# Kernel tuning notes

Hardware: AMD Instinct MI355X
Metric: run time of the kernel (lower is better)

## Reference

```python
import jax, jax.numpy as jnp
import numpy as np
from jax.scipy.linalg import expm

LATENT, HID, OMEGA, TRANZ, K = 64, 40, 9, 3, 262144


def _linear_params(key, out_d, in_d):
    # equinox Linear default init: U(-1/sqrt(in), 1/sqrt(in)) for weight and bias
    lim = 1.0 / np.sqrt(in_d)
    kw, kb = jax.random.split(key)
    W = jax.random.uniform(kw, (out_d, in_d), minval=-lim, maxval=lim, dtype=jnp.float32)
    b = jax.random.uniform(kb, (out_d,), minval=-lim, maxval=lim, dtype=jnp.float32)
    return W, b


def setup_inputs() -> dict:
    key = jax.random.key(0)
    keys = jax.random.split(key, 7)
    W_o1, b_o1 = _linear_params(keys[0], HID, LATENT)
    W_o2, b_o2 = _linear_params(keys[1], HID, HID)
    W_o3, b_o3 = _linear_params(keys[2], OMEGA, HID)
    W_t1, b_t1 = _linear_params(keys[3], HID, LATENT)
    W_t2, b_t2 = _linear_params(keys[4], HID, HID)
    W_t3, b_t3 = _linear_params(keys[5], TRANZ, HID)
    x = jax.random.normal(keys[6], (LATENT, K), dtype=jnp.float32)
    return {
        "x": x,
        "W_o1": W_o1, "b_o1": b_o1, "W_o2": W_o2, "b_o2": b_o2, "W_o3": W_o3, "b_o3": b_o3,
        "W_t1": W_t1, "b_t1": b_t1, "W_t2": W_t2, "b_t2": b_t2, "W_t3": W_t3, "b_t3": b_t3,
    }


def _exp_omega(omega_flat):
    # omega_flat: (9, K); expm of each column reshaped to 3x3, flattened -> (K, 9)
    f = lambda col: expm(col.reshape(3, 3)).reshape(9)
    return jax.vmap(f, in_axes=1)(omega_flat)


def reference(x, W_o1, b_o1, W_o2, b_o2, W_o3, b_o3,
              W_t1, b_t1, W_t2, b_t2, W_t3, b_t3):
    relu = jax.nn.relu
    # omega branch (note: original applies relu after EVERY layer, incl. last)
    h = relu(W_o1 @ x + b_o1[:, None])
    h = relu(W_o2 @ h + b_o2[:, None])
    omega = relu(W_o3 @ h + b_o3[:, None])          # (9, K)
    rotation = _exp_omega(omega).T                   # (9, K)
    # translation branch
    t = relu(W_t1 @ x + b_t1[:, None])
    t = relu(W_t2 @ t + b_t2[:, None])
    translation = relu(W_t3 @ t + b_t3[:, None])     # (3, K)
    return (omega, rotation, translation)
```

## Files before the change

### kernel.cpp

```cpp
#include <hip/hip_runtime.h>
#include <hip/hip_bf16.h>

#define KC 262144

typedef __attribute__((ext_vector_type(8))) short bf16x8;
typedef __attribute__((ext_vector_type(4))) float f32x4;
typedef unsigned short u16;
typedef unsigned int u32;

__device__ __forceinline__ u16 f2bf(float f) {
    u32 u = __float_as_uint(f);
    return (u16)((u + 0x7fffu + ((u >> 16) & 1u)) >> 16);
}
__device__ __forceinline__ u32 pk2(float a, float b) {
    u16 lo = __bfloat16_as_ushort(__float2bfloat16(a));
    u16 hi = __bfloat16_as_ushort(__float2bfloat16(b));
    return (u32)lo | ((u32)hi << 16);
}
__device__ __forceinline__ float bf2f(u32 h) {
    return __uint_as_float(h << 16);
}

__global__ __launch_bounds__(256) void prep(
    const float* __restrict__ Wo1, const float* __restrict__ bo1,
    const float* __restrict__ Wo2, const float* __restrict__ bo2,
    const float* __restrict__ Wo3, const float* __restrict__ bo3,
    const float* __restrict__ Wt1, const float* __restrict__ bt1,
    const float* __restrict__ Wt2, const float* __restrict__ bt2,
    const float* __restrict__ Wt3, const float* __restrict__ bt3,
    u16* __restrict__ ws)
{
    u16* W1s = ws;
    u16* W2s = ws + 5120;
    u16* W3s = ws + 12800;
    float* b1s = (float*)(ws + 14336);
    const int t0 = blockIdx.x * 256 + threadIdx.x;
    const int NT = gridDim.x * 256;

    for (int i = t0; i < 5120; i += NT) {
        int r = i >> 6, k = i & 63;
        float v = (r < 40) ? Wo1[r * 64 + k] : Wt1[(r - 40) * 64 + k];
        W1s[i] = f2bf(v);
    }
    for (int i = t0; i < 7680; i += NT) {
        int r = i / 96, k = i - r * 96;
        float v = 0.f;
        if (r < 40) {
            if (k < 40) v = Wo2[r * 40 + k];
            else if (k == 80) v = bo2[r];
        } else {
            int rr = r - 40;
            if (k >= 40 && k < 80) v = Wt2[rr * 40 + (k - 40)];
            else if (k == 80) v = bt2[rr];
        }
        W2s[i] = f2bf(v);
    }
    for (int i = t0; i < 1536; i += NT) {
        int r = i / 96, k = i - r * 96;
        float v = 0.f;
        if (r < 9) {
            if (k < 40) v = Wo3[r * 40 + k];
            else if (k == 80) v = bo3[r];
        } else if (r < 12) {
            int rr = r - 9;
            if (k >= 40 && k < 80) v = Wt3[rr * 40 + (k - 40)];
            else if (k == 80) v = bt3[rr];
        }
        W3s[i] = f2bf(v);
    }
    for (int i = t0; i < 80; i += NT)
        b1s[i] = (i < 40) ? bo1[i] : bt1[i - 40];
}

__device__ __forceinline__ void transpose_h(
    const u32* Px, const u32* Py, int g, int c, bf16x8* hb)
{
    const int srcA = 16 * (2 * (g & 1)) + c;
    const int srcB = srcA + 16;
    const bool hiM = (g >= 2);
#pragma unroll
    for (int s = 0; s < 2; ++s) {
        union { u32 u[4]; bf16x8 v; } uu;
        u32 a0 = (u32)__shfl((int)Px[2 * s], srcA);
        u32 b0 = (u32)__shfl((int)Px[2 * s + 1], srcA);
        uu.u[0] = hiM ? b0 : a0;
        u32 a1 = (u32)__shfl((int)Py[2 * s], srcA);
        u32 b1 = (u32)__shfl((int)Py[2 * s + 1], srcA);
        uu.u[1] = hiM ? b1 : a1;
        u32 a2 = (u32)__shfl((int)Px[2 * s], srcB);
        u32 b2 = (u32)__shfl((int)Px[2 * s + 1], srcB);
        uu.u[2] = hiM ? b2 : a2;
        u32 a3 = (u32)__shfl((int)Py[2 * s], srcB);
        u32 b3 = (u32)__shfl((int)Py[2 * s + 1], srcB);
        uu.u[3] = hiM ? b3 : a3;
        hb[s] = uu.v;
    }
    {
        union { u32 u[4]; bf16x8 v; } uu;
        u32 v0 = (u32)__shfl((int)Px[4], srcA);
        u32 v1 = (u32)__shfl((int)Py[4], srcA);
        u32 v2 = (u32)__shfl((int)Px[4], srcB);
        u32 v3 = (u32)__shfl((int)Py[4], srcB);
        u32 k0 = (g == 2) ? 0x00003f80u : 0u;
        uu.u[0] = hiM ? k0 : v0;
        uu.u[1] = hiM ? 0u : v1;
        uu.u[2] = hiM ? 0u : v2;
        uu.u[3] = hiM ? 0u : v3;
        hb[2] = uu.v;
    }
}

__global__ __launch_bounds__(256, 1) void mlp_shfl(
    const float* __restrict__ x, const u16* __restrict__ ws,
    float* __restrict__ out)
{
    const u16* W1s = ws;
    const u16* W2s = ws + 5120;
    const u16* W3s = ws + 12800;
    const float* b1s = (const float*)(ws + 14336);

    const int tid = threadIdx.x;
    const int wid = tid >> 6;
    const int lane = tid & 63;
    const int g = lane >> 4;
    const int c = lane & 15;
    const int wgid = blockIdx.x * 4 + wid;
    const int cbase = wgid * 64;

    bf16x8 A1[5][2], A3[3];
    f32x4 b1v[5];
#pragma unroll
    for (int m = 0; m < 5; ++m) {
#pragma unroll
        for (int s = 0; s < 2; ++s)
            A1[m][s] = *(const bf16x8*)(W1s + (16 * m + c) * 64 + 32 * s + 8 * g);
        b1v[m] = *(const f32x4*)(b1s + 16 * m + 4 * g);
    }
    bf16x8 A2[5][3];
#pragma unroll
    for (int m = 0; m < 5; ++m)
#pragma unroll
        for (int s = 0; s < 3; ++s)
            if (!(s == 0 && m >= 3))
                A2[m][s] = *(const bf16x8*)(W2s + (16 * m + c) * 96 + 32 * s + 8 * g);
#pragma unroll
    for (int s = 0; s < 3; ++s)
        A3[s] = *(const bf16x8*)(W3s + c * 96 + 32 * s + 8 * g);

    u32 xoff[16];
#pragma unroll
    for (int jj = 0; jj < 16; ++jj) {
        int row = 8 * g + (jj & 7) + 32 * (jj >> 3);
        xoff[jj] = (u32)((row * KC + cbase + c) * 4);
    }
    const char* xb_ = (const char*)x;

    float xr[16];
#pragma unroll
    for (int jj = 0; jj < 16; ++jj)
        xr[jj] = *(const float*)(xb_ + xoff[jj]);

    u32 w0[4], w1[4];

#pragma unroll
    for (int t = 0; t < 4; ++t) {
        bf16x8 xv[2];
#pragma unroll
        for (int s = 0; s < 2; ++s) {
            union { u32 u[4]; bf16x8 v; } uu;
#pragma unroll
            for (int p = 0; p < 4; ++p)
                uu.u[p] = pk2(xr[8 * s + 2 * p], xr[8 * s + 2 * p + 1]);
            xv[s] = uu.v;
        }

        float xrn[16];
        if (t < 3) {
#pragma unroll
            for (int jj = 0; jj < 16; ++jj)
                xrn[jj] = *(const float*)(xb_ + (xoff[jj] + (t + 1) * 64));
        }

        f32x4 a1[5];
#pragma unroll
        for (int m = 0; m < 5; ++m) a1[m] = b1v[m];
#pragma unroll
        for (int s = 0; s < 2; ++s)
#pragma unroll
            for (int m = 0; m < 5; ++m)
                a1[m] = __builtin_amdgcn_mfma_f32_16x16x32_bf16(
                    A1[m][s], xv[s], a1[m], 0, 0, 0);

        u32 Px[5], Py[5];
#pragma unroll
        for (int m = 0; m < 5; ++m) {
            Px[m] = pk2(fmaxf(a1[m][0], 0.f), fmaxf(a1[m][1], 0.f));
            Py[m] = pk2(fmaxf(a1[m][2], 0.f), fmaxf(a1[m][3], 0.f));
        }
        bf16x8 hb[3];
        transpose_h(Px, Py, g, c, hb);

        f32x4 a2[5];
#pragma unroll
        for (int m = 0; m < 5; ++m) a2[m] = f32x4{0.f, 0.f, 0.f, 0.f};
#pragma unroll
        for (int s = 0; s < 3; ++s)
#pragma unroll
            for (int m = 0; m < 5; ++m)
                if (!(s == 0 && m >= 3))
                    a2[m] = __builtin_amdgcn_mfma_f32_16x16x32_bf16(
                        A2[m][s], hb[s], a2[m], 0, 0, 0);
#pragma unroll
        for (int m = 0; m < 5; ++m) {
            Px[m] = pk2(fmaxf(a2[m][0], 0.f), fmaxf(a2[m][1], 0.f));
            Py[m] = pk2(fmaxf(a2[m][2], 0.f), fmaxf(a2[m][3], 0.f));
        }
        transpose_h(Px, Py, g, c, hb);

        f32x4 a3 = f32x4{0.f, 0.f, 0.f, 0.f};
#pragma unroll
        for (int s = 0; s < 3; ++s)
            a3 = __builtin_amdgcn_mfma_f32_16x16x32_bf16(
                A3[s], hb[s], a3, 0, 0, 0);

        w0[t] = pk2(fmaxf(a3[0], 0.f), fmaxf(a3[1], 0.f));
        w1[t] = pk2(fmaxf(a3[2], 0.f), fmaxf(a3[3], 0.f));

        if (t < 3) {
#pragma unroll
            for (int jj = 0; jj < 16; ++jj)
                xr[jj] = xrn[jj];
        }
    }

    {
        const int T = lane >> 4;
        const int cp = lane & 15;
        const int s0 = cp, s1 = 16 + cp, s2 = 32 + cp;

        auto selT = [&](u32 v0, u32 v1, u32 v2, u32 v3) -> u32 {
            u32 lo = (T & 1) ? v1 : v0;
            u32 hi = (T & 1) ? v3 : v2;
            return (T & 2) ? hi : lo;
        };
        u32 q0 = selT((u32)__shfl((int)w0[0], s0), (u32)__shfl((int)w0[1], s0),
                      (u32)__shfl((int)w0[2], s0), (u32)__shfl((int)w0[3], s0));
        u32 q1 = selT((u32)__shfl((int)w1[0], s0), (u32)__shfl((int)w1[1], s0),
                      (u32)__shfl((int)w1[2], s0), (u32)__shfl((int)w1[3], s0));
        u32 q2 = selT((u32)__shfl((int)w0[0], s1), (u32)__shfl((int)w0[1], s1),
                      (u32)__shfl((int)w0[2], s1), (u32)__shfl((int)w0[3], s1));
        u32 q3 = selT((u32)__shfl((int)w1[0], s1), (u32)__shfl((int)w1[1], s1),
                      (u32)__shfl((int)w1[2], s1), (u32)__shfl((int)w1[3], s1));
        u32 q4 = selT((u32)__shfl((int)w0[0], s2), (u32)__shfl((int)w0[1], s2),
                      (u32)__shfl((int)w0[2], s2), (u32)__shfl((int)w0[3], s2));
        u32 q5 = selT((u32)__shfl((int)w1[0], s2), (u32)__shfl((int)w1[1], s2),
                      (u32)__shfl((int)w1[2], s2), (u32)__shfl((int)w1[3], s2));

        float om[9];
        om[0] = bf2f(q0 & 0xffffu); om[1] = bf2f(q0 >> 16);
        om[2] = bf2f(q1 & 0xffffu); om[3] = bf2f(q1 >> 16);
        om[4] = bf2f(q2 & 0xffffu); om[5] = bf2f(q2 >> 16);
        om[6] = bf2f(q3 & 0xffffu); om[7] = bf2f(q3 >> 16);
        om[8] = bf2f(q4 & 0xffffu);
        float tr0 = bf2f(q4 >> 16);
        float tr1 = bf2f(q5 & 0xffffu);
        float tr2 = bf2f(q5 >> 16);

        const size_t ob = (size_t)cbase + lane;
#pragma unroll
        for (int j = 0; j < 9; ++j)
            out[(size_t)j * KC + ob] = om[j];
        out[(size_t)18 * KC + ob] = tr0;
        out[(size_t)19 * KC + ob] = tr1;
        out[(size_t)20 * KC + ob] = tr2;

        float B[9];
#pragma unroll
        for (int i = 0; i < 9; ++i) B[i] = om[i] * (1.0f / 16.0f);
        float T9[9] = {1.f, 0.f, 0.f, 0.f, 1.f, 0.f, 0.f, 0.f, 1.f};
#pragma unroll
        for (int m = 7; m >= 1; --m) {
            float U[9];
#pragma unroll
            for (int rr = 0; rr < 3; ++rr)
#pragma unroll
                for (int cc = 0; cc < 3; ++cc)
                    U[rr * 3 + cc] = B[rr * 3 + 0] * T9[0 * 3 + cc]
                                   + B[rr * 3 + 1] * T9[1 * 3 + cc]
                                   + B[rr * 3 + 2] * T9[2 * 3 + cc];
            const float s = 1.0f / (float)m;
#pragma unroll
            for (int i = 0; i < 9; ++i)
                T9[i] = U[i] * s + ((i == 0 || i == 4 || i == 8) ? 1.0f : 0.0f);
        }
#pragma unroll
        for (int q = 0; q < 4; ++q) {
            float U[9];
#pragma unroll
            for (int rr = 0; rr < 3; ++rr)
#pragma unroll
                for (int cc = 0; cc < 3; ++cc)
                    U[rr * 3 + cc] = T9[rr * 3 + 0] * T9[0 * 3 + cc]
                                   + T9[rr * 3 + 1] * T9[1 * 3 + cc]
                                   + T9[rr * 3 + 2] * T9[2 * 3 + cc];
#pragma unroll
            for (int i = 0; i < 9; ++i) T9[i] = U[i];
        }
#pragma unroll
        for (int j = 0; j < 9; ++j)
            out[(size_t)(9 + j) * KC + ob] = T9[j];
    }
}

extern "C" void kernel_launch(void* const* d_in, const int* in_sizes, int n_in,
                              void* d_out, int out_size, void* d_ws, size_t ws_size,
                              hipStream_t stream) {
    const float* x   = (const float*)d_in[0];
    const float* Wo1 = (const float*)d_in[1];
    const float* bo1 = (const float*)d_in[2];
    const float* Wo2 = (const float*)d_in[3];
    const float* bo2 = (const float*)d_in[4];
    const float* Wo3 = (const float*)d_in[5];
    const float* bo3 = (const float*)d_in[6];
    const float* Wt1 = (const float*)d_in[7];
    const float* bt1 = (const float*)d_in[8];
    const float* Wt2 = (const float*)d_in[9];
    const float* bt2 = (const float*)d_in[10];
    const float* Wt3 = (const float*)d_in[11];
    const float* bt3 = (const float*)d_in[12];

    u16* ws = (u16*)d_ws;
    float* out = (float*)d_out;

    hipLaunchKernelGGL(prep, dim3(16), dim3(256), 0, stream,
                       Wo1, bo1, Wo2, bo2, Wo3, bo3,
                       Wt1, bt1, Wt2, bt2, Wt3, bt3, ws);
    hipLaunchKernelGGL(mlp_shfl, dim3(1024), dim3(256), 0, stream,
                       x, ws, out);
}
```

Baseline: 39.24 us.

## Stage MFMA weight fragments in LDS instead of registers, raise occupancy

Prep now writes weights pre-swizzled into per-lane MFMA fragment order, and the main kernel copies them into shared memory once per block. Each MFMA then reads its A fragment from LDS instead of keeping all weight fragments live in registers. This frees many VGPRs, and the launch bound is raised to 2 blocks per CU to allow more overlap of memory latency. The cost is LDS reads inside the inner loop, an extra global-to-LDS copy with a barrier per block, and possible LDS bandwidth pressure.

```diff
diff --git a/kernel.cpp b/kernel.cpp
--- a/kernel.cpp
+++ b/kernel.cpp
@@ -19,6 +19,39 @@
 }
 __device__ __forceinline__ float bf2f(u32 h) {
     return __uint_as_float(h << 16);
+}
+
+__device__ __forceinline__ float w1elem(
+    int r, int k, const float* Wo1, const float* Wt1) {
+    return (r < 40) ? Wo1[r * 64 + k] : Wt1[(r - 40) * 64 + k];
+}
+__device__ __forceinline__ float w2elem(
+    int r, int k, const float* Wo2, const float* bo2,
+    const float* Wt2, const float* bt2) {
+    if (r < 40) {
+        if (k < 40) return Wo2[r * 40 + k];
+        if (k == 80) return bo2[r];
+        return 0.f;
+    }
+    int rr = r - 40;
+    if (k >= 40 && k < 80) return Wt2[rr * 40 + (k - 40)];
+    if (k == 80) return bt2[rr];
+    return 0.f;
+}
+__device__ __forceinline__ float w3elem(
+    int r, int k, const float* Wo3, const float* bo3,
+    const float* Wt3, const float* bt3) {
+    if (r < 9) {
+        if (k < 40) return Wo3[r * 40 + k];
+        if (k == 80) return bo3[r];
+        return 0.f;
+    }
+    if (r < 12) {
+        int rr = r - 9;
+        if (k >= 40 && k < 80) return Wt3[rr * 40 + (k - 40)];
+        if (k == 80) return bt3[rr];
+    }
+    return 0.f;
 }
 
 __global__ __launch_bounds__(256) void prep(
@@ -28,48 +61,54 @@
     const float* __restrict__ Wt1, const float* __restrict__ bt1,
     const float* __restrict__ Wt2, const float* __restrict__ bt2,
     const float* __restrict__ Wt3, const float* __restrict__ bt3,
-    u16* __restrict__ ws)
+    char* __restrict__ ws)
 {
-    u16* W1s = ws;
-    u16* W2s = ws + 5120;
-    u16* W3s = ws + 12800;
-    float* b1s = (float*)(ws + 14336);
     const int t0 = blockIdx.x * 256 + threadIdx.x;
     const int NT = gridDim.x * 256;
 
-    for (int i = t0; i < 5120; i += NT) {
-        int r = i >> 6, k = i & 63;
-        float v = (r < 40) ? Wo1[r * 64 + k] : Wt1[(r - 40) * 64 + k];
-        W1s[i] = f2bf(v);
-    }
-    for (int i = t0; i < 7680; i += NT) {
-        int r = i / 96, k = i - r * 96;
-        float v = 0.f;
-        if (r < 40) {
-            if (k < 40) v = Wo2[r * 40 + k];
-            else if (k == 80) v = bo2[r];
+    for (int i = t0; i < 26 * 64; i += NT) {
+        const int f = i >> 6, l = i & 63;
+        const int g = l >> 4, c = l & 15;
+        u16 v[8];
+        if (f < 10) {
+            const int m = f >> 1, s = f & 1;
+#pragma unroll
+            for (int e = 0; e < 8; ++e)
+                v[e] = f2bf(w1elem(16 * m + c, 32 * s + 8 * g + e, Wo1, Wt1));
+        } else if (f < 23) {
+            const int q = f - 10;
+            const int s = (q < 3) ? 0 : (q < 8) ? 1 : 2;
+            const int m = (q < 3) ? q : (q < 8) ? q - 3 : q - 8;
+#pragma unroll
+            for (int e = 0; e < 8; ++e)
+                v[e] = f2bf(w2elem(16 * m + c, 32 * s + 8 * g + e,
+                                   Wo2, bo2, Wt2, bt2));
         } else {
-            int rr = r - 40;
-            if (k >= 40 && k < 80) v = Wt2[rr * 40 + (k - 40)];
-            else if (k == 80) v = bt2[rr];
-        }
-        W2s[i] = f2bf(v);
-    }
-    for (int i = t0; i < 1536; i += NT) {
-        int r = i / 96, k = i - r * 96;
-        float v = 0.f;
-        if (r < 9) {
-            if (k < 40) v = Wo3[r * 40 + k];
-            else if (k == 80) v = bo3[r];
-        } else if (r < 12) {
-            int rr = r - 9;
-            if (k >= 40 && k < 80) v = Wt3[rr * 40 + (k - 40)];
-            else if (k == 80) v = bt3[rr];
-        }
-        W3s[i] = f2bf(v);
-    }
-    for (int i = t0; i < 80; i += NT)
-        b1s[i] = (i < 40) ? bo1[i] : bt1[i - 40];
+            const int s = f - 23;
+#pragma unroll
+            for (int e = 0; e < 8; ++e)
+                v[e] = f2bf(w3elem(c, 32 * s + 8 * g + e, Wo3, bo3, Wt3, bt3));
+        }
+        uint4 pk;
+        pk.x = (u32)v[0] | ((u32)v[1] << 16);
+        pk.y = (u32)v[2] | ((u32)v[3] << 16);
+        pk.z = (u32)v[4] | ((u32)v[5] << 16);
+        pk.w = (u32)v[6] | ((u32)v[7] << 16);
+        *(uint4*)(ws + (size_t)i * 16) = pk;
+    }
+
+    for (int i = t0; i < 5 * 64; i += NT) {
+        const int m = i >> 6, l = i & 63;
+        const int g = l >> 4;
+        float v[4];
+#pragma unroll
+        for (int j = 0; j < 4; ++j) {
+            const int idx = 16 * m + 4 * g + j;
+            v[j] = (idx < 40) ? bo1[idx] : bt1[idx - 40];
+        }
+        *(float4*)(ws + 26624 + (size_t)i * 16) =
+            make_float4(v[0], v[1], v[2], v[3]);
+    }
 }
 
 __device__ __forceinline__ void transpose_h(
@@ -110,14 +149,12 @@
     }
 }
 
-__global__ __launch_bounds__(256, 1) void mlp_shfl(
-    const float* __restrict__ x, const u16* __restrict__ ws,
+__global__ __launch_bounds__(256, 2) void mlp_wlds(
+    const float* __restrict__ x, const char* __restrict__ ws,
     float* __restrict__ out)
 {
-    const u16* W1s = ws;
-    const u16* W2s = ws + 5120;
-    const u16* W3s = ws + 12800;
-    const float* b1s = (const float*)(ws + 14336);
+    __shared__ uint4 wlds4[1984];
+    char* wlds = (char*)wlds4;
 
     const int tid = threadIdx.x;
     const int wid = tid >> 6;
@@ -127,25 +164,15 @@
     const int wgid = blockIdx.x * 4 + wid;
     const int cbase = wgid * 64;
 
-    bf16x8 A1[5][2], A3[3];
+    for (int i = tid; i < 1984; i += 256)
+        wlds4[i] = ((const uint4*)ws)[i];
+    __syncthreads();
+
+    const int lb = lane * 16;
     f32x4 b1v[5];
 #pragma unroll
-    for (int m = 0; m < 5; ++m) {
-#pragma unroll
-        for (int s = 0; s < 2; ++s)
-            A1[m][s] = *(const bf16x8*)(W1s + (16 * m + c) * 64 + 32 * s + 8 * g);
-        b1v[m] = *(const f32x4*)(b1s + 16 * m + 4 * g);
-    }
-    bf16x8 A2[5][3];
-#pragma unroll
     for (int m = 0; m < 5; ++m)
-#pragma unroll
-        for (int s = 0; s < 3; ++s)
-            if (!(s == 0 && m >= 3))
-                A2[m][s] = *(const bf16x8*)(W2s + (16 * m + c) * 96 + 32 * s + 8 * g);
-#pragma unroll
-    for (int s = 0; s < 3; ++s)
-        A3[s] = *(const bf16x8*)(W3s + c * 96 + 32 * s + 8 * g);
+        b1v[m] = *(const f32x4*)(wlds + 26624 + m * 1024 + lb);
 
     u32 xoff[16];
 #pragma unroll
@@ -187,9 +214,11 @@
 #pragma unroll
         for (int s = 0; s < 2; ++s)
 #pragma unroll
-            for (int m = 0; m < 5; ++m)
+            for (int m = 0; m < 5; ++m) {
+                bf16x8 af = *(const bf16x8*)(wlds + (m * 2 + s) * 1024 + lb);
                 a1[m] = __builtin_amdgcn_mfma_f32_16x16x32_bf16(
-                    A1[m][s], xv[s], a1[m], 0, 0, 0);
+                    af, xv[s], a1[m], 0, 0, 0);
+            }
 
         u32 Px[5], Py[5];
 #pragma unroll
@@ -206,10 +235,13 @@
 #pragma unroll
         for (int s = 0; s < 3; ++s)
 #pragma unroll
-            for (int m = 0; m < 5; ++m)
-                if (!(s == 0 && m >= 3))
-                    a2[m] = __builtin_amdgcn_mfma_f32_16x16x32_bf16(
-                        A2[m][s], hb[s], a2[m], 0, 0, 0);
+            for (int m = 0; m < 5; ++m) {
+                if (s == 0 && m >= 3) continue;
+                const int q = (s == 0) ? m : (s == 1) ? 3 + m : 8 + m;
+                bf16x8 af = *(const bf16x8*)(wlds + (10 + q) * 1024 + lb);
+                a2[m] = __builtin_amdgcn_mfma_f32_16x16x32_bf16(
+                    af, hb[s], a2[m], 0, 0, 0);
+            }
 #pragma unroll
         for (int m = 0; m < 5; ++m) {
             Px[m] = pk2(fmaxf(a2[m][0], 0.f), fmaxf(a2[m][1], 0.f));
@@ -219,9 +251,11 @@
 
         f32x4 a3 = f32x4{0.f, 0.f, 0.f, 0.f};
 #pragma unroll
-        for (int s = 0; s < 3; ++s)
+        for (int s = 0; s < 3; ++s) {
+            bf16x8 af = *(const bf16x8*)(wlds + (23 + s) * 1024 + lb);
             a3 = __builtin_amdgcn_mfma_f32_16x16x32_bf16(
-                A3[s], hb[s], a3, 0, 0, 0);
+                af, hb[s], a3, 0, 0, 0);
+        }
 
         w0[t] = pk2(fmaxf(a3[0], 0.f), fmaxf(a3[1], 0.f));
         w1[t] = pk2(fmaxf(a3[2], 0.f), fmaxf(a3[3], 0.f));
@@ -329,12 +363,12 @@
     const float* Wt3 = (const float*)d_in[11];
     const float* bt3 = (const float*)d_in[12];
 
-    u16* ws = (u16*)d_ws;
+    char* ws = (char*)d_ws;
     float* out = (float*)d_out;
 
-    hipLaunchKernelGGL(prep, dim3(16), dim3(256), 0, stream,
+    hipLaunchKernelGGL(prep, dim3(8), dim3(256), 0, stream,
                        Wo1, bo1, Wo2, bo2, Wo3, bo3,
                        Wt1, bt1, Wt2, bt2, Wt3, bt3, ws);
-    hipLaunchKernelGGL(mlp_shfl, dim3(1024), dim3(256), 0, stream,
+    hipLaunchKernelGGL(mlp_wlds, dim3(1024), dim3(256), 0, stream,
                        x, ws, out);
 }
```

After: 35.18 us. -10.3%, faster.
